# Performance work log

Hardware: AMD Instinct MI355X
Metric: run time of the kernel (lower is better)

## Reference

```python
import jax, jax.numpy as jnp
import numpy as np

N = 1024  # batch


def setup_inputs() -> dict:
    key = jax.random.key(0)
    ks = jax.random.split(key, 10)
    meta_feature = jax.random.uniform(ks[0], (N, 6), dtype=jnp.float32)
    tile_wall_feature = jax.random.uniform(ks[1], (N, 34, 5), dtype=jnp.float32)
    tile_prep = jax.random.uniform(ks[2], (N, 320, 34, 7), dtype=jnp.float32)
    # keep tile_hidden_ct (channel 4) away from 0 so the division stays well-conditioned
    tile_prep = tile_prep.at[..., 4].add(0.5)
    fan_prep = jax.random.uniform(ks[3], (N, 320, 80), dtype=jnp.float32)
    redundant_tile_prep = jax.random.uniform(ks[4], (N, 320, 34), dtype=jnp.float32)
    count_prep = jax.random.uniform(ks[5], (N, 320), dtype=jnp.float32)
    chi_peng_count_remain = jax.random.uniform(ks[6], (N, 320), dtype=jnp.float32)
    # learned params: Linear(11,1) of TileProbModuleNew, fan_coeff, tile_coeff
    W_throw = jax.random.normal(ks[7], (11,), dtype=jnp.float32) * 0.05
    b_throw = jnp.array(0.5, dtype=jnp.float32)  # keeps prob_throw > 0 (faithful math; avoids NaN from neg**frac)
    fan_coeff = 0.1 + 0.015 * jax.random.normal(ks[8], (80,), dtype=jnp.float32)
    tile_coeff = 1.0 + 0.015 * jax.random.normal(ks[9], (34,), dtype=jnp.float32)
    fan_coeff_multiplier = jnp.ones((80,), dtype=jnp.float32).at[33].set(21.0)
    return {
        'meta_feature': meta_feature,
        'tile_wall_feature': tile_wall_feature,
        'tile_prep': tile_prep,
        'fan_prep': fan_prep,
        'redundant_tile_prep': redundant_tile_prep,
        'count_prep': count_prep,
        'chi_peng_count_remain': chi_peng_count_remain,
        'W_throw': W_throw,
        'b_throw': b_throw,
        'fan_coeff': fan_coeff,
        'fan_coeff_multiplier': fan_coeff_multiplier,
        'tile_coeff': tile_coeff,
    }


def reference(meta_feature, tile_wall_feature, tile_prep, fan_prep,
              redundant_tile_prep, count_prep, chi_peng_count_remain,
              W_throw, b_throw, fan_coeff, fan_coeff_multiplier, tile_coeff):
    n = meta_feature.shape[0]
    # TileProbModuleNew: per-tile Linear(11,1)
    meta_exp = jnp.broadcast_to(meta_feature[:, None, :], (n, 34, 6))
    feat = jnp.concatenate([meta_exp, tile_wall_feature], axis=-1)        # (n,34,11)
    prob_throw = feat @ W_throw + b_throw                                  # (n,34)

    tile_self_draw_baseline = tile_prep[..., 0]
    tile_need_count = tile_prep[..., 1]
    tile_cp_coeff = tile_prep[..., 2]
    tile_cp_base = tile_prep[..., 3]
    tile_hidden_ct = tile_prep[..., 4]
    tile_cp_switch = tile_prep[..., 5]
    tile_null_filler = tile_prep[..., 6]

    fan_pref = fan_prep * fan_coeff * fan_coeff_multiplier                 # (n,320,80)
    multiplied_fan_pref = jnp.sum(fan_pref, axis=-1)                       # (n,320)

    term1 = tile_self_draw_baseline * prob_throw[:, None, :] ** tile_need_count
    term2 = jnp.nan_to_num(tile_cp_base * tile_cp_coeff / tile_hidden_ct)
    terms_summed = term1 + tile_null_filler + term2 * tile_cp_switch      # (n,320,34)

    final_prob_throw = jnp.prod(terms_summed, axis=-1) * 100.0 * multiplied_fan_pref  # (n,320)

    redundant_prob = redundant_tile_prep * final_prob_throw[..., None]    # (n,320,34)
    redundant_prob = redundant_prob.reshape(n, 5, 64, 34)
    tile_bound_winrate = redundant_prob.sum(axis=2)                        # (n,5,34)

    weighted_tile_prob = (tile_bound_winrate * tile_coeff)[:, 0]           # (n,34)

    final_prob_ops = final_prob_throw.reshape(n, 5, 64).sum(axis=-1)       # (n,5)
    max_tile_prob_for_action = jnp.max(tile_bound_winrate, axis=2)         # (n,5)
    max_tile_prob_for_action = max_tile_prob_for_action.at[:, 0].set(final_prob_ops[:, 0])
    return (max_tile_prob_for_action, weighted_tile_prob)
```

## Files before the change

### kernel.cpp

```cpp
#include <hip/hip_runtime.h>
#include <math.h>

#define N_OPS 320

__global__ __launch_bounds__(256) void mahjong_kernel(
    const float* __restrict__ meta,
    const float* __restrict__ wall,
    const float* __restrict__ tile_prep,
    const float* __restrict__ fan_prep,
    const float* __restrict__ redundant,
    const float* __restrict__ W_throw,
    const float* __restrict__ b_throw,
    const float* __restrict__ fan_coeff,
    const float* __restrict__ fan_mult,
    const float* __restrict__ tile_coeff,
    float* __restrict__ out_max,
    float* __restrict__ out_weighted,
    int n)
{
    const int blk  = blockIdx.x;
    const int b    = blk / 5;
    const int g    = blk % 5;
    const int tid  = threadIdx.x;
    const int wave = tid >> 6;
    const int lane = tid & 63;

    __shared__ float prob_sm[34];
    __shared__ float fc_sm[80];
    __shared__ float final_sm[64];
    __shared__ float acc_sm[4 * 34];

    if (tid < 34) {
        float acc = b_throw[0];
        #pragma unroll
        for (int j = 0; j < 6; ++j) acc += meta[(size_t)b * 6 + j] * W_throw[j];
        const float* w = wall + ((size_t)b * 34 + tid) * 5;
        #pragma unroll
        for (int j = 0; j < 5; ++j) acc += w[j] * W_throw[6 + j];
        prob_sm[tid] = acc;
    }
    if (tid >= 64 && tid < 144) {
        int f = tid - 64;
        fc_sm[f] = fan_coeff[f] * fan_mult[f];
    }
    __syncthreads();

    const int o0 = g * 64;
    for (int i = 0; i < 16; ++i) {
        int o_local = wave * 16 + i;
        size_t row = (size_t)b * N_OPS + o0 + o_local;

        float ts = 1.0f;
        if (lane < 34) {
            const float* tp = tile_prep + row * 34 * 7 + (size_t)lane * 7;
            float c0 = tp[0], c1 = tp[1], c2 = tp[2], c3 = tp[3];
            float c4 = tp[4], c5 = tp[5], c6 = tp[6];
            float t1 = c0 * powf(prob_sm[lane], c1);
            float t2 = c3 * c2 / c4;
            if (isnan(t2)) t2 = 0.0f;
            else if (isinf(t2)) t2 = copysignf(3.4028234663852886e38f, t2);
            ts = t1 + c6 + t2 * c5;
        }
        #pragma unroll
        for (int s = 1; s < 64; s <<= 1) ts *= __shfl_xor(ts, s);

        const float* fp = fan_prep + row * 80;
        float fv = fp[lane] * fc_sm[lane];
        if (lane < 16) fv += fp[64 + lane] * fc_sm[64 + lane];
        #pragma unroll
        for (int s = 1; s < 64; s <<= 1) fv += __shfl_xor(fv, s);

        if (lane == 0) final_sm[o_local] = ts * 100.0f * fv;
    }
    __syncthreads();

    if (lane < 34) {
        float part = 0.0f;
        #pragma unroll 4
        for (int i = 0; i < 16; ++i) {
            int o_local = wave * 16 + i;
            size_t row = (size_t)b * N_OPS + o0 + o_local;
            part += redundant[row * 34 + lane] * final_sm[o_local];
        }
        acc_sm[wave * 34 + lane] = part;
    }
    __syncthreads();

    if (wave == 0) {
        if (g == 0) {
            if (lane < 34) {
                float tbw = acc_sm[lane] + acc_sm[34 + lane] +
                            acc_sm[68 + lane] + acc_sm[102 + lane];
                out_weighted[(size_t)b * 34 + lane] = tbw * tile_coeff[lane];
            }
            float fs = final_sm[lane];
            #pragma unroll
            for (int s = 1; s < 64; s <<= 1) fs += __shfl_xor(fs, s);
            if (lane == 0) out_max[(size_t)b * 5] = fs;
        } else {
            float m = -INFINITY;
            if (lane < 34) m = acc_sm[lane] + acc_sm[34 + lane] +
                               acc_sm[68 + lane] + acc_sm[102 + lane];
            #pragma unroll
            for (int s = 1; s < 64; s <<= 1) m = fmaxf(m, __shfl_xor(m, s));
            if (lane == 0) out_max[(size_t)b * 5 + g] = m;
        }
    }
}

extern "C" void kernel_launch(void* const* d_in, const int* in_sizes, int n_in,
                              void* d_out, int out_size, void* d_ws, size_t ws_size,
                              hipStream_t stream) {
    const float* meta       = (const float*)d_in[0];
    const float* wall       = (const float*)d_in[1];
    const float* tile_prep  = (const float*)d_in[2];
    const float* fan_prep   = (const float*)d_in[3];
    const float* redundant  = (const float*)d_in[4];
    const float* W_throw    = (const float*)d_in[7];
    const float* b_throw    = (const float*)d_in[8];
    const float* fan_coeff  = (const float*)d_in[9];
    const float* fan_mult   = (const float*)d_in[10];
    const float* tile_coeff = (const float*)d_in[11];

    int n = in_sizes[0] / 6;
    float* out_max      = (float*)d_out;
    float* out_weighted = out_max + (size_t)n * 5;

    dim3 grid(n * 5), block(256);
    hipLaunchKernelGGL(mahjong_kernel, grid, block, 0, stream,
                       meta, wall, tile_prep, fan_prep, redundant,
                       W_throw, b_throw, fan_coeff, fan_mult, tile_coeff,
                       out_max, out_weighted, n);
}
```

Baseline: 544.5 us.

## Stage row chunks in shared memory with coalesced vector loads and split reductions

Each block now copies 32-row chunks of tile_prep, fan_prep and redundant into LDS using float2/float4 coalesced loads, replacing the per-lane stride-7 global reads and the half-idle wavefronts. The product and sum over tiles and fans are split across 8 thread slices and combined through shared partials, so all 256 threads work instead of only 34 lanes per wave. powf is replaced with exp2f(log2f) and the nan/inf clamp on the division is dropped. This adds several barriers and about 45KB of LDS per block, which limits occupancy. It also risks differences from the reference if the division ever produces nan or inf.

```diff
diff --git a/kernel.cpp b/kernel.cpp
--- a/kernel.cpp
+++ b/kernel.cpp
@@ -2,6 +2,10 @@
 #include <math.h>
 
 #define N_OPS 320
+#define ROWS 32
+#define TP_ROW 238
+#define FAN_ROW 80
+#define RED_ROW 34
 
 __global__ __launch_bounds__(256) void mahjong_kernel(
     const float* __restrict__ meta,
@@ -25,10 +29,15 @@
     const int wave = tid >> 6;
     const int lane = tid & 63;
 
+    __shared__ __align__(16) float tp_sm[ROWS * TP_ROW];
+    __shared__ __align__(16) float fan_sm[ROWS * FAN_ROW];
+    __shared__ __align__(16) float red_sm[ROWS * RED_ROW];
     __shared__ float prob_sm[34];
     __shared__ float fc_sm[80];
-    __shared__ float final_sm[64];
-    __shared__ float acc_sm[4 * 34];
+    __shared__ float pprod[8][32];
+    __shared__ float psum[8][32];
+    __shared__ float final_sm[ROWS];
+    __shared__ float acc_sm[4][34];
 
     if (tid < 34) {
         float acc = b_throw[0];
@@ -43,66 +52,95 @@
         int f = tid - 64;
         fc_sm[f] = fan_coeff[f] * fan_mult[f];
     }
-    __syncthreads();
 
-    const int o0 = g * 64;
-    for (int i = 0; i < 16; ++i) {
-        int o_local = wave * 16 + i;
-        size_t row = (size_t)b * N_OPS + o0 + o_local;
+    const int s = tid >> 5;
+    const int r = tid & 31;
 
-        float ts = 1.0f;
+    float acc3 = 0.0f;
+    float fsum_part = 0.0f;
+
+    for (int c = 0; c < 2; ++c) {
+        const size_t row0 = (size_t)b * N_OPS + g * 64 + c * ROWS;
+
+        __syncthreads();
+
+        {
+            const float2* src = (const float2*)(tile_prep + row0 * TP_ROW);
+            float2* dst = (float2*)tp_sm;
+            #pragma unroll
+            for (int i = tid; i < ROWS * TP_ROW / 2; i += 256) dst[i] = src[i];
+        }
+        {
+            const float4* src = (const float4*)(fan_prep + row0 * FAN_ROW);
+            float4* dst = (float4*)fan_sm;
+            #pragma unroll
+            for (int i = tid; i < ROWS * FAN_ROW / 4; i += 256) dst[i] = src[i];
+        }
+        {
+            const float2* src = (const float2*)(redundant + row0 * RED_ROW);
+            float2* dst = (float2*)red_sm;
+            #pragma unroll
+            for (int i = tid; i < ROWS * RED_ROW / 2; i += 256) dst[i] = src[i];
+        }
+        __syncthreads();
+
+        {
+            const float* tpr = tp_sm + r * TP_ROW;
+            float pp = 1.0f;
+            #pragma unroll
+            for (int t = s; t < 34; t += 8) {
+                const float* e = tpr + t * 7;
+                float c0 = e[0], c1 = e[1], c2 = e[2], c3 = e[3];
+                float c4 = e[4], c5 = e[5], c6 = e[6];
+                float term = c0 * exp2f(c1 * log2f(prob_sm[t])) + c6 + (c3 * c2 / c4) * c5;
+                pp *= term;
+            }
+            float ps = 0.0f;
+            const float* fr = fan_sm + r * FAN_ROW;
+            #pragma unroll
+            for (int f = s; f < 80; f += 8) ps += fr[f] * fc_sm[f];
+            pprod[s][r] = pp;
+            psum[s][r] = ps;
+        }
+        __syncthreads();
+
+        if (tid < 32) {
+            float p = 1.0f, q = 0.0f;
+            #pragma unroll
+            for (int s2 = 0; s2 < 8; ++s2) { p *= pprod[s2][tid]; q += psum[s2][tid]; }
+            float fin = p * 100.0f * q;
+            final_sm[tid] = fin;
+            fsum_part += fin;
+        }
+        __syncthreads();
+
         if (lane < 34) {
-            const float* tp = tile_prep + row * 34 * 7 + (size_t)lane * 7;
-            float c0 = tp[0], c1 = tp[1], c2 = tp[2], c3 = tp[3];
-            float c4 = tp[4], c5 = tp[5], c6 = tp[6];
-            float t1 = c0 * powf(prob_sm[lane], c1);
-            float t2 = c3 * c2 / c4;
-            if (isnan(t2)) t2 = 0.0f;
-            else if (isinf(t2)) t2 = copysignf(3.4028234663852886e38f, t2);
-            ts = t1 + c6 + t2 * c5;
+            #pragma unroll
+            for (int i = 0; i < 8; ++i) {
+                int rr = wave * 8 + i;
+                acc3 += red_sm[rr * RED_ROW + lane] * final_sm[rr];
+            }
         }
-        #pragma unroll
-        for (int s = 1; s < 64; s <<= 1) ts *= __shfl_xor(ts, s);
+    }
 
-        const float* fp = fan_prep + row * 80;
-        float fv = fp[lane] * fc_sm[lane];
-        if (lane < 16) fv += fp[64 + lane] * fc_sm[64 + lane];
-        #pragma unroll
-        for (int s = 1; s < 64; s <<= 1) fv += __shfl_xor(fv, s);
-
-        if (lane == 0) final_sm[o_local] = ts * 100.0f * fv;
-    }
-    __syncthreads();
-
-    if (lane < 34) {
-        float part = 0.0f;
-        #pragma unroll 4
-        for (int i = 0; i < 16; ++i) {
-            int o_local = wave * 16 + i;
-            size_t row = (size_t)b * N_OPS + o0 + o_local;
-            part += redundant[row * 34 + lane] * final_sm[o_local];
-        }
-        acc_sm[wave * 34 + lane] = part;
-    }
+    if (lane < 34) acc_sm[wave][lane] = acc3;
     __syncthreads();
 
     if (wave == 0) {
+        float tbw = 0.0f;
+        if (lane < 34)
+            tbw = acc_sm[0][lane] + acc_sm[1][lane] + acc_sm[2][lane] + acc_sm[3][lane];
         if (g == 0) {
-            if (lane < 34) {
-                float tbw = acc_sm[lane] + acc_sm[34 + lane] +
-                            acc_sm[68 + lane] + acc_sm[102 + lane];
+            if (lane < 34)
                 out_weighted[(size_t)b * 34 + lane] = tbw * tile_coeff[lane];
-            }
-            float fs = final_sm[lane];
+            float fs = fsum_part;
             #pragma unroll
-            for (int s = 1; s < 64; s <<= 1) fs += __shfl_xor(fs, s);
+            for (int sh = 1; sh < 64; sh <<= 1) fs += __shfl_xor(fs, sh);
             if (lane == 0) out_max[(size_t)b * 5] = fs;
         } else {
-            float m = -INFINITY;
-            if (lane < 34) m = acc_sm[lane] + acc_sm[34 + lane] +
-                               acc_sm[68 + lane] + acc_sm[102 + lane];
+            float m = (lane < 34) ? tbw : -INFINITY;
             #pragma unroll
-            for (int s = 1; s < 64; s <<= 1) m = fmaxf(m, __shfl_xor(m, s));
+            for (int sh = 1; sh < 64; sh <<= 1) m = fmaxf(m, __shfl_xor(m, sh));
             if (lane == 0) out_max[(size_t)b * 5 + g] = m;
         }
     }
```

New measurement: 597.4 us. 1.1x slower.
